# Kernel tuning notes

Measured on AMD Instinct MI355X. Metric: run time of the kernel, lower is better.

The kernel has to match this reference:

```python
import jax, jax.numpy as jnp
import numpy as np

TEMPERATURE = 1.0
TOP_K = 50
TOP_P = 0.95
NEG_INF = float('-inf')


def setup_inputs() -> dict:
    key = jax.random.key(0)
    k1, k2, k3, k4 = jax.random.split(key, 4)
    B, S, D, V = 32, 8, 1024, 50257
    psi_real = jax.random.normal(k1, (B, S, D), dtype=jnp.float32)
    psi_imag = jax.random.normal(k2, (B, S, D), dtype=jnp.float32)
    W_real = jax.random.normal(k3, (V, D), dtype=jnp.float32) * 0.02
    W_imag = jax.random.normal(k4, (V, D), dtype=jnp.float32) * 0.02
    bias = jnp.zeros((V,), dtype=jnp.float32)
    return {"psi_real": psi_real, "psi_imag": psi_imag, "W_real": W_real,
            "W_imag": W_imag, "bias": bias}


def _legacy_filter(logits, temperature, top_k, top_p):
    # temperature
    l = logits / max(temperature, 1e-8)
    # top-k: keep values >= k-th largest
    if 0 < top_k < l.shape[-1]:
        topk_vals = jax.lax.top_k(l, top_k)[0]          # [B,S,k]
        threshold = topk_vals[..., -1:]
        l = jnp.where(l < threshold, NEG_INF, l)
    # top-p (nucleus): mask tokens where exclusive cumulative prob >= p
    if top_p < 1.0:
        p = max(top_p, 1e-6)
        order = jnp.argsort(-l, axis=-1)                # descending
        sl = jnp.take_along_axis(l, order, axis=-1)
        sp = jax.nn.softmax(sl, axis=-1)
        cum = jnp.cumsum(sp, axis=-1)
        mask = (cum - sp) >= p                          # exclusive cumsum >= p
        mask = mask.at[..., 0].set(False)               # always keep top token
        sl = jnp.where(mask, NEG_INF, sl)
        inv = jnp.argsort(order, axis=-1)               # scatter back to original order
        l = jnp.take_along_axis(sl, inv, axis=-1)
    return l


def reference(psi_real, psi_imag, W_real, W_imag, bias):
    # logits = proj_real(psi.real) + proj_imag(psi.imag) + bias  -> [B,S,V]
    logits = (jnp.einsum('bsd,vd->bsv', psi_real, W_real)
              + jnp.einsum('bsd,vd->bsv', psi_imag, W_imag) + bias)
    sampling_logits = _legacy_filter(logits, TEMPERATURE, TOP_K, TOP_P)
    probs = jax.nn.softmax(sampling_logits, axis=-1)
    # multinomial(probs, 1) == categorical over filtered logits
    tokens = jax.random.categorical(jax.random.key(42), sampling_logits, axis=-1)
    log_probs = jax.nn.log_softmax(logits, axis=-1)
    return logits, tokens, probs, log_probs
```

## Files before the change

### kernel.cpp

```cpp
#include <hip/hip_runtime.h>
#include <stdint.h>
#include <math.h>

#define MM 256
#define KD 1024
#define K2 2048
#define VV 50257
#define NF4 (VV / 4)
#define NSTEP 32

static constexpr size_t OUT_TOKENS = (size_t)MM * VV;
static constexpr size_t OUT_PROBS  = OUT_TOKENS + MM;
static constexpr size_t OUT_LOGPR  = OUT_PROBS + (size_t)MM * VV;

#define WS_ABUF_BYTES (2u * 1024u * 1024u)

typedef __attribute__((ext_vector_type(8))) short bf16x8;
typedef __attribute__((ext_vector_type(4))) float f32x4;

__device__ __forceinline__ ushort f2bf(float x) {
  unsigned u = __float_as_uint(x);
  unsigned r = u + 0x7FFFu + ((u >> 16) & 1u);
  return (ushort)(r >> 16);
}
__device__ __forceinline__ float bf2f(ushort h) {
  return __uint_as_float(((unsigned)h) << 16);
}

__device__ __forceinline__ unsigned rotl32(unsigned x, int r) {
  return (x << r) | (x >> (32 - r));
}

__device__ __forceinline__ uint2 threefry2x32(unsigned k0, unsigned k1,
                                              unsigned x0, unsigned x1) {
  unsigned ks[3] = {k0, k1, k0 ^ k1 ^ 0x1BD11BDAu};
  const int rot[8] = {13, 15, 26, 6, 17, 29, 16, 24};
  x0 += ks[0]; x1 += ks[1];
  #pragma unroll
  for (int g = 0; g < 5; ++g) {
    const int base = (g & 1) ? 4 : 0;
    #pragma unroll
    for (int i = 0; i < 4; ++i) {
      x0 += x1;
      x1 = rotl32(x1, rot[base + i]);
      x1 ^= x0;
    }
    x0 += ks[(g + 1) % 3];
    x1 += ks[(g + 2) % 3] + (unsigned)(g + 1);
  }
  return make_uint2(x0, x1);
}

__device__ __forceinline__ float gumbel_at(unsigned flat) {
  uint2 r = threefry2x32(0u, 42u, 0u, flat);
  unsigned w = r.x ^ r.y;
  unsigned fb = (w >> 9) | 0x3F800000u;
  float f = __uint_as_float(fb) - 1.0f;
  const float tiny = 1.1754943508222875e-38f;
  float u = fmaxf(tiny, f + tiny);
  float t1 = (float)log((double)u);
  float t3 = (float)log((double)(-t1));
  return -t3;
}

__global__ __launch_bounds__(256)
void k_prep(const float* __restrict__ psi_r, const float* __restrict__ psi_i,
            ushort* __restrict__ a_buf) {
  int t = blockIdx.x * 256 + threadIdx.x;
  int lane = t & 63;
  int mb = (t >> 6) & 15;
  int s = t >> 10;
  int lr = lane & 15, lg = lane >> 4;
  int m = mb * 16 + lr;
  int kloc = (s & 31) * 32 + lg * 8;
  const float* __restrict__ src = (s < 32) ? psi_r : psi_i;
  float4 v0 = *reinterpret_cast<const float4*>(&src[m * KD + kloc]);
  float4 v1 = *reinterpret_cast<const float4*>(&src[m * KD + kloc + 4]);
  float in[8] = {v0.x, v0.y, v0.z, v0.w, v1.x, v1.y, v1.z, v1.w};
  ushort h[8], l[8];
  #pragma unroll
  for (int j = 0; j < 8; ++j) {
    h[j] = f2bf(in[j]);
    l[j] = f2bf(in[j] - bf2f(h[j]));
  }
  size_t base = ((size_t)(s * 16 + mb) * 2) * 512 + (size_t)lane * 8;
  #pragma unroll
  for (int j = 0; j < 8; ++j) {
    a_buf[base + j] = h[j];
    a_buf[base + 512 + j] = l[j];
  }
}

#define BN 64
#define BK 64
#define GT 256

struct W4 { float4 a, b, c, d; };
struct A8 { uint4 h[4]; uint4 l[4]; };

__device__ __forceinline__ void loadW(W4& w, const float* __restrict__ Wr,
                                      const float* __restrict__ Wi,
                                      int t, int gn, int bcol) {
  const float* __restrict__ Bs = (t < 16) ? Wr : Wi;
  int ko = (t << 6) & (KD - 1);
  if (gn < VV) {
    const float* p = &Bs[(size_t)gn * KD + ko + bcol];
    w.a = *reinterpret_cast<const float4*>(p);
    w.b = *reinterpret_cast<const float4*>(p + 4);
    w.c = *reinterpret_cast<const float4*>(p + 8);
    w.d = *reinterpret_cast<const float4*>(p + 12);
  }
}

__device__ __forceinline__ void stageW(const W4& w, ushort* __restrict__ bh,
                                       ushort* __restrict__ bl, int eo0, int eo1) {
  float in[16] = {w.a.x, w.a.y, w.a.z, w.a.w, w.b.x, w.b.y, w.b.z, w.b.w,
                  w.c.x, w.c.y, w.c.z, w.c.w, w.d.x, w.d.y, w.d.z, w.d.w};
  ushort h[16], l[16];
  #pragma unroll
  for (int j = 0; j < 16; ++j) {
    h[j] = f2bf(in[j]);
    l[j] = f2bf(in[j] - bf2f(h[j]));
  }
  *reinterpret_cast<uint4*>(&bh[eo0]) =
      make_uint4((unsigned)h[0] | ((unsigned)h[1] << 16),
                 (unsigned)h[2] | ((unsigned)h[3] << 16),
                 (unsigned)h[4] | ((unsigned)h[5] << 16),
                 (unsigned)h[6] | ((unsigned)h[7] << 16));
  *reinterpret_cast<uint4*>(&bh[eo1]) =
      make_uint4((unsigned)h[8] | ((unsigned)h[9] << 16),
                 (unsigned)h[10] | ((unsigned)h[11] << 16),
                 (unsigned)h[12] | ((unsigned)h[13] << 16),
                 (unsigned)h[14] | ((unsigned)h[15] << 16));
  *reinterpret_cast<uint4*>(&bl[eo0]) =
      make_uint4((unsigned)l[0] | ((unsigned)l[1] << 16),
                 (unsigned)l[2] | ((unsigned)l[3] << 16),
                 (unsigned)l[4] | ((unsigned)l[5] << 16),
                 (unsigned)l[6] | ((unsigned)l[7] << 16));
  *reinterpret_cast<uint4*>(&bl[eo1]) =
      make_uint4((unsigned)l[8] | ((unsigned)l[9] << 16),
                 (unsigned)l[10] | ((unsigned)l[11] << 16),
                 (unsigned)l[12] | ((unsigned)l[13] << 16),
                 (unsigned)l[14] | ((unsigned)l[15] << 16));
}

__device__ __forceinline__ void loadA(A8& A, const uint4* __restrict__ a_buf,
                                      int s, int kq, int wid, int lane) {
  #pragma unroll
  for (int mi = 0; mi < 4; ++mi) {
    int chunk2 = (((s * 2 + kq) * 16) + wid * 4 + mi) * 2;
    A.h[mi] = a_buf[(size_t)chunk2 * 64 + lane];
    A.l[mi] = a_buf[(size_t)(chunk2 + 1) * 64 + lane];
  }
}

__device__ __forceinline__ void computeKQ(f32x4 (&acc)[4][4], const A8& A,
                                          const ushort* __restrict__ bhp,
                                          const ushort* __restrict__ blp,
                                          int kq, int lr, int lg) {
  bf16x8 bh[4], bl[4];
  #pragma unroll
  for (int ni = 0; ni < 4; ++ni) {
    int r = ni * 16 + lr;
    int eoff = r * BK + ((kq * 32 + lg * 8) ^ ((r & 7) << 3));
    bh[ni] = *reinterpret_cast<const bf16x8*>(&bhp[eoff]);
    bl[ni] = *reinterpret_cast<const bf16x8*>(&blp[eoff]);
  }
  __builtin_amdgcn_s_setprio(1);
  #pragma unroll
  for (int mi = 0; mi < 4; ++mi) {
    bf16x8 ah = *reinterpret_cast<const bf16x8*>(&A.h[mi]);
    bf16x8 al = *reinterpret_cast<const bf16x8*>(&A.l[mi]);
    #pragma unroll
    for (int ni = 0; ni < 4; ++ni) {
      acc[mi][ni] = __builtin_amdgcn_mfma_f32_16x16x32_bf16(ah, bh[ni], acc[mi][ni], 0, 0, 0);
      acc[mi][ni] = __builtin_amdgcn_mfma_f32_16x16x32_bf16(al, bh[ni], acc[mi][ni], 0, 0, 0);
      acc[mi][ni] = __builtin_amdgcn_mfma_f32_16x16x32_bf16(ah, bl[ni], acc[mi][ni], 0, 0, 0);
    }
  }
  __builtin_amdgcn_s_setprio(0);
}

__global__ __launch_bounds__(GT, 2)
void k_gemm(const uint4* __restrict__ a_buf,
            const float* __restrict__ Wr, const float* __restrict__ Wi,
            const float* __restrict__ bias, float* __restrict__ logits) {
  __shared__ ushort sBh[2][BN * BK];
  __shared__ ushort sBl[2][BN * BK];

  const int tid  = threadIdx.x;
  const int lane = tid & 63;
  const int wid  = tid >> 6;
  const int vb   = blockIdx.x * BN;
  const int lr = lane & 15;
  const int lg = lane >> 4;

  const int brow = tid >> 2;
  const int bcol = (tid & 3) << 4;
  const int gn   = vb + brow;
  const int eo0  = brow * BK + (bcol ^ ((brow & 7) << 3));
  const int eo1  = brow * BK + ((bcol + 8) ^ ((brow & 7) << 3));

  f32x4 acc[4][4];
  #pragma unroll
  for (int i = 0; i < 4; ++i)
    #pragma unroll
    for (int j = 0; j < 4; ++j)
      #pragma unroll
      for (int q = 0; q < 4; ++q) acc[i][j][q] = 0.f;

  W4 wX, wY;
  wX.a = wX.b = wX.c = wX.d = make_float4(0.f, 0.f, 0.f, 0.f);
  wY = wX;
  A8 A0, A1;
  loadW(wX, Wr, Wi, 0, gn, bcol);
  loadW(wY, Wr, Wi, 1, gn, bcol);
  loadA(A0, a_buf, 0, 0, wid, lane);
  stageW(wX, &sBh[0][0], &sBl[0][0], eo0, eo1);
  loadW(wX, Wr, Wi, 2, gn, bcol);
  asm volatile("s_waitcnt lgkmcnt(0)" ::: "memory");
  asm volatile("s_barrier" ::: "memory");

  for (int sp = 0; sp < NSTEP / 2; ++sp) {
    const int s0 = sp * 2;
    const int s1 = s0 + 1;
    loadA(A1, a_buf, s0, 1, wid, lane);
    stageW(wY, &sBh[1][0], &sBl[1][0], eo0, eo1);
    if (s0 + 3 < NSTEP) loadW(wY, Wr, Wi, s0 + 3, gn, bcol);
    computeKQ(acc, A0, &sBh[0][0], &sBl[0][0], 0, lr, lg);
    loadA(A0, a_buf, s1, 0, wid, lane);
    computeKQ(acc, A1, &sBh[0][0], &sBl[0][0], 1, lr, lg);
    asm volatile("s_waitcnt lgkmcnt(0)" ::: "memory");
    asm volatile("s_barrier" ::: "memory");
    loadA(A1, a_buf, s1, 1, wid, lane);
    if (s1 + 1 < NSTEP) stageW(wX, &sBh[0][0], &sBl[0][0], eo0, eo1);
    if (s1 + 3 < NSTEP) loadW(wX, Wr, Wi, s1 + 3, gn, bcol);
    computeKQ(acc, A0, &sBh[1][0], &sBl[1][0], 0, lr, lg);
    if (s1 < NSTEP - 1) loadA(A0, a_buf, s1 + 1, 0, wid, lane);
    computeKQ(acc, A1, &sBh[1][0], &sBl[1][0], 1, lr, lg);
    asm volatile("s_waitcnt lgkmcnt(0)" ::: "memory");
    asm volatile("s_barrier" ::: "memory");
  }

  #pragma unroll
  for (int ni = 0; ni < 4; ++ni) {
    int n = vb + ni * 16 + lr;
    if (n < VV) {
      float b = bias[n];
      #pragma unroll
      for (int mi = 0; mi < 4; ++mi) {
        #pragma unroll
        for (int j = 0; j < 4; ++j) {
          int m = wid * 64 + mi * 16 + lg * 4 + j;
          logits[(size_t)m * VV + n] = acc[mi][ni][j] + b;
        }
      }
    }
  }
}

__device__ __forceinline__ unsigned ordf(float f) {
  unsigned u = __float_as_uint(f);
  return u ^ ((u >> 31) ? 0xFFFFFFFFu : 0x80000000u);
}

#define HREP 4
#define HSTRIDE 4097

__global__ __launch_bounds__(1024)
void k_stats(const float* __restrict__ logits, float* __restrict__ ws4) {
  const int row = blockIdx.x;
  const int tid = threadIdx.x;
  const float* __restrict__ x = logits + (size_t)row * VV;

  __shared__ unsigned hist[HREP * HSTRIDE];
  __shared__ float pm[16], ps[16];

  for (int i = tid; i < HREP * HSTRIDE; i += 1024) hist[i] = 0u;
  __syncthreads();

  const int rep = (tid & 3) * HSTRIDE;
  float lm = -INFINITY, ls = 0.f;
  for (int i4 = tid; i4 < NF4; i4 += 1024) {
    float4 v4 = *reinterpret_cast<const float4*>(&x[i4 * 4]);
    float vs[4] = {v4.x, v4.y, v4.z, v4.w};
    #pragma unroll
    for (int j = 0; j < 4; ++j) {
      float v = vs[j];
      atomicAdd(&hist[rep + (ordf(v) >> 20)], 1u);
      if (v <= lm) {
        ls += expf(v - lm);
      } else {
        ls = ls * expf(lm - v) + 1.f;
        lm = v;
      }
    }
  }
  if (tid == 0) {
    float v = x[VV - 1];
    atomicAdd(&hist[ordf(v) >> 20], 1u);
    if (v <= lm) ls += expf(v - lm);
    else { ls = ls * expf(lm - v) + 1.f; lm = v; }
  }
  #pragma unroll
  for (int off = 32; off; off >>= 1) {
    float om = __shfl_xor(lm, off);
    float os = __shfl_xor(ls, off);
    float M = fmaxf(lm, om);
    ls = ls * expf(lm - M) + os * expf(om - M);
    lm = M;
  }
  if ((tid & 63) == 0) { pm[tid >> 6] = lm; ps[tid >> 6] = ls; }
  __syncthreads();

  for (int b = tid; b < 4096; b += 1024)
    hist[b] = hist[b] + hist[HSTRIDE + b] + hist[2 * HSTRIDE + b] + hist[3 * HSTRIDE + b];
  __syncthreads();

  if (tid < 64) {
    float m2 = (tid < 16) ? pm[tid] : -3e38f;
    float s2 = (tid < 16) ? ps[tid] : 0.f;
    #pragma unroll
    for (int off = 8; off; off >>= 1) {
      float om = __shfl_xor(m2, off);
      float os = __shfl_xor(s2, off);
      float M = fmaxf(m2, om);
      s2 = s2 * expf(m2 - M) + os * expf(om - M);
      m2 = M;
    }
    unsigned seg = 0;
    #pragma unroll 8
    for (int b = 0; b < 64; ++b) seg += hist[tid * 64 + ((b + tid) & 63)];
    unsigned suf = seg;
    #pragma unroll
    for (int off = 1; off < 64; off <<= 1) {
      unsigned o = __shfl_down(suf, off);
      if (tid + off < 64) suf += o;
    }
    unsigned long long mk = __ballot(suf >= 50u);
    int lstar = 63 - __builtin_clzll(mk);
    unsigned above = (lstar < 63) ? (unsigned)__shfl((int)suf, lstar + 1) : 0u;
    if (tid == 0) {
      unsigned cum = above;
      int bin = lstar * 64;
      for (int b = 63; b >= 0; --b) {
        cum += hist[lstar * 64 + b];
        if (cum >= 50u) { bin = lstar * 64 + b; break; }
      }
      ws4[row * 4 + 0] = m2;
      ws4[row * 4 + 1] = logf(s2);
      ws4[row * 4 + 2] = __uint_as_float((unsigned)bin << 20);
    }
  }
}

#define CAP 1024

__global__ __launch_bounds__(1024)
void k_post(const float* __restrict__ logits, const float* __restrict__ ws4,
            float* __restrict__ logpr, float* __restrict__ probs,
            float* __restrict__ tokens) {
  const int row = blockIdx.x;
  const int tid = threadIdx.x;
  const float* __restrict__ x = logits + (size_t)row * VV;
  float* __restrict__ lp = logpr + (size_t)row * VV;
  float* __restrict__ pr = probs + (size_t)row * VV;

  __shared__ float cv[CAP];
  __shared__ int   ci[CAP];
  __shared__ unsigned s_cnt;
  __shared__ float top_v[50];
  __shared__ int   top_i[50];

  if (tid == 0) s_cnt = 0u;
  __syncthreads();

  const float mx = ws4[row * 4 + 0];
  const float lz = ws4[row * 4 + 1];
  const unsigned lo = __float_as_uint(ws4[row * 4 + 2]);
  const float4 z4 = make_float4(0.f, 0.f, 0.f, 0.f);

  for (int i4 = tid; i4 < NF4; i4 += 1024) {
    float4 v = *reinterpret_cast<const float4*>(&x[i4 * 4]);
    *reinterpret_cast<float4*>(&lp[i4 * 4]) =
        make_float4((v.x - mx) - lz, (v.y - mx) - lz,
                    (v.z - mx) - lz, (v.w - mx) - lz);
    *reinterpret_cast<float4*>(&pr[i4 * 4]) = z4;
    float vs[4] = {v.x, v.y, v.z, v.w};
    #pragma unroll
    for (int j = 0; j < 4; ++j) {
      if (ordf(vs[j]) >= lo) {
        unsigned pos = atomicAdd(&s_cnt, 1u);
        if (pos < CAP) { cv[pos] = vs[j]; ci[pos] = i4 * 4 + j; }
      }
    }
  }
  if (tid == 0) {
    float v = x[VV - 1];
    lp[VV - 1] = (v - mx) - lz;
    pr[VV - 1] = 0.f;
    if (ordf(v) >= lo) {
      unsigned pos = atomicAdd(&s_cnt, 1u);
      if (pos < CAP) { cv[pos] = v; ci[pos] = VV - 1; }
    }
  }
  __syncthreads();
  const int ncand = (int)min(s_cnt, (unsigned)CAP);

  if (tid < 64) {
    for (int it = 0; it < 50; ++it) {
      float bv = -INFINITY;
      int bi = 0x7FFFFFFF, bs = 0;
      for (int c = tid; c < ncand; c += 64) {
        float v = cv[c];
        int id = ci[c];
        if (v > bv || (v == bv && id < bi)) { bv = v; bi = id; bs = c; }
      }
      #pragma unroll
      for (int off = 32; off; off >>= 1) {
        float ov = __shfl_xor(bv, off);
        int oi = __shfl_xor(bi, off);
        int os = __shfl_xor(bs, off);
        if (ov > bv || (ov == bv && oi < bi)) { bv = ov; bi = oi; bs = os; }
      }
      if (tid == 0) {
        top_v[it] = bv;
        top_i[it] = bi;
        cv[bs] = -INFINITY;
      }
    }

    float tv = (tid < 50) ? top_v[tid] : -3e38f;
    float m0 = top_v[0];
    float sp = (tid < 50) ? expf(tv - m0) : 0.f;
    float Z = sp;
    #pragma unroll
    for (int off = 32; off; off >>= 1) Z += __shfl_xor(Z, off);
    float pref = sp;
    #pragma unroll
    for (int off = 1; off < 64; off <<= 1) {
      float o = __shfl_up(pref, off);
      if (tid >= off) pref += o;
    }
    float excl = (pref - sp) / Z;
    bool keep = (tid < 50) && ((tid == 0) || (excl < 0.95f));
    float spk = keep ? sp : 0.f;
    float Z2 = spk;
    #pragma unroll
    for (int off = 32; off; off >>= 1) Z2 += __shfl_xor(Z2, off);

    float bt = -3e38f;
    int bidx = 0x7FFFFFFF;
    if (keep) {
      int idx = top_i[tid];
      pr[idx] = sp / Z2;
      bt = tv + gumbel_at((unsigned)((size_t)row * VV + idx));
      bidx = idx;
    }
    #pragma unroll
    for (int off = 32; off; off >>= 1) {
      float ot = __shfl_xor(bt, off);
      int oi = __shfl_xor(bidx, off);
      if (ot > bt || (ot == bt && oi < bidx)) { bt = ot; bidx = oi; }
    }
    if (tid == 0) tokens[row] = (float)bidx;
  }
}

extern "C" void kernel_launch(void* const* d_in, const int* in_sizes, int n_in,
                              void* d_out, int out_size, void* d_ws, size_t ws_size,
                              hipStream_t stream) {
  const float* psi_r = (const float*)d_in[0];
  const float* psi_i = (const float*)d_in[1];
  const float* Wr    = (const float*)d_in[2];
  const float* Wi    = (const float*)d_in[3];
  const float* bias  = (const float*)d_in[4];
  float* out = (float*)d_out;

  ushort* a_buf = (ushort*)d_ws;
  float* ws4    = (float*)((char*)d_ws + WS_ABUF_BYTES);

  float* logits = out;
  float* tokens = out + OUT_TOKENS;
  float* probs  = out + OUT_PROBS;
  float* logpr  = out + OUT_LOGPR;

  k_prep<<<256, 256, 0, stream>>>(psi_r, psi_i, a_buf);
  const int nblk = (VV + BN - 1) / BN;
  k_gemm<<<nblk, GT, 0, stream>>>((const uint4*)a_buf, Wr, Wi, bias, logits);
  k_stats<<<MM, 1024, 0, stream>>>(logits, ws4);
  k_post<<<MM, 1024, 0, stream>>>(logits, ws4, logpr, probs, tokens);
}
```

Baseline: 284.1 us.

## Use single-pass fp16 MFMA GEMM and recompute top candidates exactly in fp64

Replaces the split-bf16 (hi/lo, three MFMAs per tile) GEMM with a single fp16 MFMA pass, which removes two thirds of the matrix work, half the staging traffic and the lo-part conversions. Because fp16 logits are less accurate, the top-k threshold bin is widened by one bin. The post kernel selects 56 candidates and recomputes their logits exactly with fp64 dot products against W before re-sorting and sampling. The risk is that the logits and log_probs outputs now carry fp16-level error, and fp16 can overflow or underflow on inputs outside the test range.

```diff
diff --git a/kernel.cpp b/kernel.cpp
--- a/kernel.cpp
+++ b/kernel.cpp
@@ -13,19 +13,10 @@
 static constexpr size_t OUT_PROBS  = OUT_TOKENS + MM;
 static constexpr size_t OUT_LOGPR  = OUT_PROBS + (size_t)MM * VV;
 
-#define WS_ABUF_BYTES (2u * 1024u * 1024u)
-
-typedef __attribute__((ext_vector_type(8))) short bf16x8;
+#define WS_ABUF_BYTES (1u * 1024u * 1024u)
+
+typedef __attribute__((ext_vector_type(8))) _Float16 f16x8;
 typedef __attribute__((ext_vector_type(4))) float f32x4;
-
-__device__ __forceinline__ ushort f2bf(float x) {
-  unsigned u = __float_as_uint(x);
-  unsigned r = u + 0x7FFFu + ((u >> 16) & 1u);
-  return (ushort)(r >> 16);
-}
-__device__ __forceinline__ float bf2f(ushort h) {
-  return __uint_as_float(((unsigned)h) << 16);
-}
 
 __device__ __forceinline__ unsigned rotl32(unsigned x, int r) {
   return (x << r) | (x >> (32 - r));
@@ -77,18 +68,11 @@
   float4 v0 = *reinterpret_cast<const float4*>(&src[m * KD + kloc]);
   float4 v1 = *reinterpret_cast<const float4*>(&src[m * KD + kloc + 4]);
   float in[8] = {v0.x, v0.y, v0.z, v0.w, v1.x, v1.y, v1.z, v1.w};
-  ushort h[8], l[8];
-  #pragma unroll
-  for (int j = 0; j < 8; ++j) {
-    h[j] = f2bf(in[j]);
-    l[j] = f2bf(in[j] - bf2f(h[j]));
-  }
-  size_t base = ((size_t)(s * 16 + mb) * 2) * 512 + (size_t)lane * 8;
-  #pragma unroll
-  for (int j = 0; j < 8; ++j) {
-    a_buf[base + j] = h[j];
-    a_buf[base + 512 + j] = l[j];
-  }
+  _Float16 h[8];
+  #pragma unroll
+  for (int j = 0; j < 8; ++j) h[j] = (_Float16)in[j];
+  size_t base = (size_t)(s * 16 + mb) * 512 + (size_t)lane * 8;
+  *reinterpret_cast<uint4*>(&a_buf[base]) = *reinterpret_cast<uint4*>(h);
 }
 
 #define BN 64
@@ -96,7 +80,7 @@
 #define GT 256
 
 struct W4 { float4 a, b, c, d; };
-struct A8 { uint4 h[4]; uint4 l[4]; };
+struct A4 { uint4 h[4]; };
 
 __device__ __forceinline__ void loadW(W4& w, const float* __restrict__ Wr,
                                       const float* __restrict__ Wi,
@@ -113,70 +97,42 @@
 }
 
 __device__ __forceinline__ void stageW(const W4& w, ushort* __restrict__ bh,
-                                       ushort* __restrict__ bl, int eo0, int eo1) {
+                                       int eo0, int eo1) {
   float in[16] = {w.a.x, w.a.y, w.a.z, w.a.w, w.b.x, w.b.y, w.b.z, w.b.w,
                   w.c.x, w.c.y, w.c.z, w.c.w, w.d.x, w.d.y, w.d.z, w.d.w};
-  ushort h[16], l[16];
-  #pragma unroll
-  for (int j = 0; j < 16; ++j) {
-    h[j] = f2bf(in[j]);
-    l[j] = f2bf(in[j] - bf2f(h[j]));
-  }
-  *reinterpret_cast<uint4*>(&bh[eo0]) =
-      make_uint4((unsigned)h[0] | ((unsigned)h[1] << 16),
-                 (unsigned)h[2] | ((unsigned)h[3] << 16),
-                 (unsigned)h[4] | ((unsigned)h[5] << 16),
-                 (unsigned)h[6] | ((unsigned)h[7] << 16));
-  *reinterpret_cast<uint4*>(&bh[eo1]) =
-      make_uint4((unsigned)h[8] | ((unsigned)h[9] << 16),
-                 (unsigned)h[10] | ((unsigned)h[11] << 16),
-                 (unsigned)h[12] | ((unsigned)h[13] << 16),
-                 (unsigned)h[14] | ((unsigned)h[15] << 16));
-  *reinterpret_cast<uint4*>(&bl[eo0]) =
-      make_uint4((unsigned)l[0] | ((unsigned)l[1] << 16),
-                 (unsigned)l[2] | ((unsigned)l[3] << 16),
-                 (unsigned)l[4] | ((unsigned)l[5] << 16),
-                 (unsigned)l[6] | ((unsigned)l[7] << 16));
-  *reinterpret_cast<uint4*>(&bl[eo1]) =
-      make_uint4((unsigned)l[8] | ((unsigned)l[9] << 16),
-                 (unsigned)l[10] | ((unsigned)l[11] << 16),
-                 (unsigned)l[12] | ((unsigned)l[13] << 16),
-                 (unsigned)l[14] | ((unsigned)l[15] << 16));
-}
-
-__device__ __forceinline__ void loadA(A8& A, const uint4* __restrict__ a_buf,
+  _Float16 h[16];
+  #pragma unroll
+  for (int j = 0; j < 16; ++j) h[j] = (_Float16)in[j];
+  *reinterpret_cast<uint4*>(&bh[eo0]) = reinterpret_cast<uint4*>(h)[0];
+  *reinterpret_cast<uint4*>(&bh[eo1]) = reinterpret_cast<uint4*>(h)[1];
+}
+
+__device__ __forceinline__ void loadA(A4& A, const uint4* __restrict__ a_buf,
                                       int s, int kq, int wid, int lane) {
   #pragma unroll
   for (int mi = 0; mi < 4; ++mi) {
-    int chunk2 = (((s * 2 + kq) * 16) + wid * 4 + mi) * 2;
-    A.h[mi] = a_buf[(size_t)chunk2 * 64 + lane];
-    A.l[mi] = a_buf[(size_t)(chunk2 + 1) * 64 + lane];
-  }
-}
-
-__device__ __forceinline__ void computeKQ(f32x4 (&acc)[4][4], const A8& A,
+    int chunk = ((s * 2 + kq) * 16) + wid * 4 + mi;
+    A.h[mi] = a_buf[(size_t)chunk * 64 + lane];
+  }
+}
+
+__device__ __forceinline__ void computeKQ(f32x4 (&acc)[4][4], const A4& A,
                                           const ushort* __restrict__ bhp,
-                                          const ushort* __restrict__ blp,
                                           int kq, int lr, int lg) {
-  bf16x8 bh[4], bl[4];
+  f16x8 bh[4];
   #pragma unroll
   for (int ni = 0; ni < 4; ++ni) {
     int r = ni * 16 + lr;
     int eoff = r * BK + ((kq * 32 + lg * 8) ^ ((r & 7) << 3));
-    bh[ni] = *reinterpret_cast<const bf16x8*>(&bhp[eoff]);
-    bl[ni] = *reinterpret_cast<const bf16x8*>(&blp[eoff]);
+    bh[ni] = *reinterpret_cast<const f16x8*>(&bhp[eoff]);
   }
   __builtin_amdgcn_s_setprio(1);
   #pragma unroll
   for (int mi = 0; mi < 4; ++mi) {
-    bf16x8 ah = *reinterpret_cast<const bf16x8*>(&A.h[mi]);
-    bf16x8 al = *reinterpret_cast<const bf16x8*>(&A.l[mi]);
-    #pragma unroll
-    for (int ni = 0; ni < 4; ++ni) {
-      acc[mi][ni] = __builtin_amdgcn_mfma_f32_16x16x32_bf16(ah, bh[ni], acc[mi][ni], 0, 0, 0);
-      acc[mi][ni] = __builtin_amdgcn_mfma_f32_16x16x32_bf16(al, bh[ni], acc[mi][ni], 0, 0, 0);
-      acc[mi][ni] = __builtin_amdgcn_mfma_f32_16x16x32_bf16(ah, bl[ni], acc[mi][ni], 0, 0, 0);
-    }
+    f16x8 ah = *reinterpret_cast<const f16x8*>(&A.h[mi]);
+    #pragma unroll
+    for (int ni = 0; ni < 4; ++ni)
+      acc[mi][ni] = __builtin_amdgcn_mfma_f32_16x16x32_f16(ah, bh[ni], acc[mi][ni], 0, 0, 0);
   }
   __builtin_amdgcn_s_setprio(0);
 }
@@ -185,8 +141,7 @@
 void k_gemm(const uint4* __restrict__ a_buf,
             const float* __restrict__ Wr, const float* __restrict__ Wi,
             const float* __restrict__ bias, float* __restrict__ logits) {
-  __shared__ ushort sBh[2][BN * BK];
-  __shared__ ushort sBl[2][BN * BK];
+  __shared__ ushort sB[2][BN * BK];
 
   const int tid  = threadIdx.x;
   const int lane = tid & 63;
@@ -212,11 +167,11 @@
   W4 wX, wY;
   wX.a = wX.b = wX.c = wX.d = make_float4(0.f, 0.f, 0.f, 0.f);
   wY = wX;
-  A8 A0, A1;
+  A4 A0, A1;
   loadW(wX, Wr, Wi, 0, gn, bcol);
   loadW(wY, Wr, Wi, 1, gn, bcol);
   loadA(A0, a_buf, 0, 0, wid, lane);
-  stageW(wX, &sBh[0][0], &sBl[0][0], eo0, eo1);
+  stageW(wX, &sB[0][0], eo0, eo1);
   loadW(wX, Wr, Wi, 2, gn, bcol);
   asm volatile("s_waitcnt lgkmcnt(0)" ::: "memory");
   asm volatile("s_barrier" ::: "memory");
@@ -225,19 +180,19 @@
     const int s0 = sp * 2;
     const int s1 = s0 + 1;
     loadA(A1, a_buf, s0, 1, wid, lane);
-    stageW(wY, &sBh[1][0], &sBl[1][0], eo0, eo1);
+    stageW(wY, &sB[1][0], eo0, eo1);
     if (s0 + 3 < NSTEP) loadW(wY, Wr, Wi, s0 + 3, gn, bcol);
-    computeKQ(acc, A0, &sBh[0][0], &sBl[0][0], 0, lr, lg);
+    computeKQ(acc, A0, &sB[0][0], 0, lr, lg);
     loadA(A0, a_buf, s1, 0, wid, lane);
-    computeKQ(acc, A1, &sBh[0][0], &sBl[0][0], 1, lr, lg);
+    computeKQ(acc, A1, &sB[0][0], 1, lr, lg);
     asm volatile("s_waitcnt lgkmcnt(0)" ::: "memory");
     asm volatile("s_barrier" ::: "memory");
     loadA(A1, a_buf, s1, 1, wid, lane);
-    if (s1 + 1 < NSTEP) stageW(wX, &sBh[0][0], &sBl[0][0], eo0, eo1);
+    if (s1 + 1 < NSTEP) stageW(wX, &sB[0][0], eo0, eo1);
     if (s1 + 3 < NSTEP) loadW(wX, Wr, Wi, s1 + 3, gn, bcol);
-    computeKQ(acc, A0, &sBh[1][0], &sBl[1][0], 0, lr, lg);
+    computeKQ(acc, A0, &sB[1][0], 0, lr, lg);
     if (s1 < NSTEP - 1) loadA(A0, a_buf, s1 + 1, 0, wid, lane);
-    computeKQ(acc, A1, &sBh[1][0], &sBl[1][0], 1, lr, lg);
+    computeKQ(acc, A1, &sB[1][0], 1, lr, lg);
     asm volatile("s_waitcnt lgkmcnt(0)" ::: "memory");
     asm volatile("s_barrier" ::: "memory");
   }
@@ -347,6 +302,7 @@
         cum += hist[lstar * 64 + b];
         if (cum >= 50u) { bin = lstar * 64 + b; break; }
       }
+      bin = (bin > 0) ? bin - 1 : 0;
       ws4[row * 4 + 0] = m2;
       ws4[row * 4 + 1] = logf(s2);
       ws4[row * 4 + 2] = __uint_as_float((unsigned)bin << 20);
@@ -355,9 +311,13 @@
 }
 
 #define CAP 1024
+#define NSEL 56
 
 __global__ __launch_bounds__(1024)
 void k_post(const float* __restrict__ logits, const float* __restrict__ ws4,
+            const float* __restrict__ psi_r, const float* __restrict__ psi_i,
+            const float* __restrict__ Wr, const float* __restrict__ Wi,
+            const float* __restrict__ bias,
             float* __restrict__ logpr, float* __restrict__ probs,
             float* __restrict__ tokens) {
   const int row = blockIdx.x;
@@ -369,8 +329,11 @@
   __shared__ float cv[CAP];
   __shared__ int   ci[CAP];
   __shared__ unsigned s_cnt;
-  __shared__ float top_v[50];
-  __shared__ int   top_i[50];
+  __shared__ float top_v[NSEL];
+  __shared__ int   top_i[NSEL];
+  __shared__ float srt_v[50];
+  __shared__ int   srt_i[50];
+  __shared__ int   s_nsel;
 
   if (tid == 0) s_cnt = 0u;
   __syncthreads();
@@ -408,7 +371,7 @@
   const int ncand = (int)min(s_cnt, (unsigned)CAP);
 
   if (tid < 64) {
-    for (int it = 0; it < 50; ++it) {
+    for (int it = 0; it < NSEL; ++it) {
       float bv = -INFINITY;
       int bi = 0x7FFFFFFF, bs = 0;
       for (int c = tid; c < ncand; c += 64) {
@@ -429,9 +392,53 @@
         cv[bs] = -INFINITY;
       }
     }
-
-    float tv = (tid < 50) ? top_v[tid] : -3e38f;
-    float m0 = top_v[0];
+    if (tid == 0) s_nsel = (ncand < NSEL) ? ncand : NSEL;
+  }
+  __syncthreads();
+  const int nsel = s_nsel;
+
+  {
+    const int wv = tid >> 6, ln = tid & 63;
+    const float* __restrict__ prr = psi_r + (size_t)row * KD;
+    const float* __restrict__ pii = psi_i + (size_t)row * KD;
+    for (int j = wv; j < nsel; j += 16) {
+      int idx = top_i[j];
+      const float* __restrict__ wr = Wr + (size_t)idx * KD;
+      const float* __restrict__ wi = Wi + (size_t)idx * KD;
+      double ar = 0.0, ai = 0.0;
+      for (int k = ln; k < KD; k += 64) {
+        ar += (double)prr[k] * (double)wr[k];
+        ai += (double)pii[k] * (double)wi[k];
+      }
+      #pragma unroll
+      for (int off = 32; off; off >>= 1) {
+        ar += __shfl_xor(ar, off);
+        ai += __shfl_xor(ai, off);
+      }
+      if (ln == 0) top_v[j] = ((float)ar + (float)ai) + bias[idx];
+    }
+  }
+  __syncthreads();
+
+  if (tid < 64) {
+    float v = (tid < nsel) ? top_v[tid] : -INFINITY;
+    int id = (tid < nsel) ? top_i[tid] : 0x7FFFFFFF;
+    for (int it = 0; it < 50; ++it) {
+      float bv = v;
+      int bi = id, bl = tid;
+      #pragma unroll
+      for (int off = 32; off; off >>= 1) {
+        float ov = __shfl_xor(bv, off);
+        int oi = __shfl_xor(bi, off);
+        int ol = __shfl_xor(bl, off);
+        if (ov > bv || (ov == bv && oi < bi)) { bv = ov; bi = oi; bl = ol; }
+      }
+      if (tid == 0) { srt_v[it] = bv; srt_i[it] = bi; }
+      if (tid == bl) { v = -INFINITY; id = 0x7FFFFFFF; }
+    }
+
+    float tv = (tid < 50) ? srt_v[tid] : -3e38f;
+    float m0 = srt_v[0];
     float sp = (tid < 50) ? expf(tv - m0) : 0.f;
     float Z = sp;
     #pragma unroll
@@ -452,7 +459,7 @@
     float bt = -3e38f;
     int bidx = 0x7FFFFFFF;
     if (keep) {
-      int idx = top_i[tid];
+      int idx = srt_i[tid];
       pr[idx] = sp / Z2;
       bt = tv + gumbel_at((unsigned)((size_t)row * VV + idx));
       bidx = idx;
@@ -489,5 +496,6 @@
   const int nblk = (VV + BN - 1) / BN;
   k_gemm<<<nblk, GT, 0, stream>>>((const uint4*)a_buf, Wr, Wi, bias, logits);
   k_stats<<<MM, 1024, 0, stream>>>(logits, ws4);
-  k_post<<<MM, 1024, 0, stream>>>(logits, ws4, logpr, probs, tokens);
-}
+  k_post<<<MM, 1024, 0, stream>>>(logits, ws4, psi_r, psi_i, Wr, Wi, bias,
+                                  logpr, probs, tokens);
+}
```

After: 323.8 us, median of 3. 14.0% more time.
